# Optimization experiments

Measured on AMD Instinct MI355X. Metric: run time of the kernel, lower is better.

Reference implementation:

```python
import jax, jax.numpy as jnp
import numpy as np

MESSAGE_PASSES = 3  # constants.message_passes
F_NODE = 64   # hidden_node_features
F_EDGE = 16   # n_edge_features
M_MSG = 64    # message_size
OUT_DIM = 128
B, N = 8, 256
EDGE_DENSITY = 0.1


def setup_inputs() -> dict:
    key = jax.random.key(0)
    ks = jax.random.split(key, 12)
    nodes = jax.random.normal(ks[0], (B, N, F_NODE), dtype=jnp.float32)
    # sparse positive edge features: rand * bernoulli connectivity (avg degree ~ N*density)
    raw = jax.random.uniform(ks[1], (B, N, N, F_EDGE), dtype=jnp.float32)
    conn = (jax.random.uniform(ks[2], (B, N, N)) < EDGE_DENSITY).astype(jnp.float32)
    edges = raw * conn[..., None]
    s = 0.05
    return {
        "nodes": nodes,
        "edges": edges,
        # message MLP: cat(neighbour, edge) -> message_size
        "W_msg": jax.random.normal(ks[3], (F_NODE + F_EDGE, M_MSG), dtype=jnp.float32) * s,
        "b_msg": jnp.zeros((M_MSG,), dtype=jnp.float32),
        # GRU cell (input=message_size, hidden=F_NODE), gates [r|z|n]
        "W_i": jax.random.normal(ks[4], (M_MSG, 3 * F_NODE), dtype=jnp.float32) * s,
        "W_h": jax.random.normal(ks[5], (F_NODE, 3 * F_NODE), dtype=jnp.float32) * s,
        "b_i": jnp.zeros((3 * F_NODE,), dtype=jnp.float32),
        "b_h": jnp.zeros((3 * F_NODE,), dtype=jnp.float32),
        # gated readout
        "W_g": jax.random.normal(ks[6], (2 * F_NODE, OUT_DIM), dtype=jnp.float32) * s,
        "b_g": jnp.zeros((OUT_DIM,), dtype=jnp.float32),
        "W_e": jax.random.normal(ks[7], (F_NODE, OUT_DIM), dtype=jnp.float32) * s,
        "b_e": jnp.zeros((OUT_DIM,), dtype=jnp.float32),
    }


def reference(nodes, edges, W_msg, b_msg, W_i, W_h, b_i, b_h, W_g, b_g, W_e, b_e):
    # adjacency[b,i,j] != 0  <=>  edge (i<-j) exists (original: edges.sum(3).nonzero)
    adjacency = edges.sum(axis=-1)                                   # (B,N,N)
    nbr_mask = (adjacency != 0).astype(nodes.dtype)                  # (B,N,N)
    node_mask = (adjacency.sum(axis=-1) != 0)                        # (B,N) bool
    node_mask_f = node_mask.astype(nodes.dtype)

    h = nodes                                                        # hidden_nodes init = nodes
    b, n, f = nodes.shape
    for _ in range(MESSAGE_PASSES):
        # message_terms over all (node i, neighbour j) pairs; masked sum == padded-gather sum
        nghb = jnp.broadcast_to(h[:, None, :, :], (b, n, n, f))      # (B,N,N,F) neighbour feats
        feat = jnp.concatenate([nghb, edges], axis=-1)               # (B,N,N,F+E)
        terms = jax.nn.relu(feat @ W_msg + b_msg)                    # (B,N,N,M)
        messages = jnp.einsum('bijm,bij->bim', terms, nbr_mask)      # summation aggregation
        # GRU cell update
        gi = messages @ W_i + b_i                                    # (B,N,3F)
        gh = h @ W_h + b_h
        ir, iz, inn = jnp.split(gi, 3, axis=-1)
        hr, hz, hn = jnp.split(gh, 3, axis=-1)
        r = jax.nn.sigmoid(ir + hr)
        z = jax.nn.sigmoid(iz + hz)
        ng = jnp.tanh(inn + r * hn)
        h_new = (1.0 - z) * ng + z * h
        # only nodes with nonzero degree are scattered back (original indexes node_batch idc)
        h = jnp.where(node_mask[..., None], h_new, h)

    # gated readout: sum_i mask_i * sigmoid(g([h_i, x_i])) * e(h_i)
    gate = jax.nn.sigmoid(jnp.concatenate([h, nodes], axis=-1) @ W_g + b_g)  # (B,N,OUT)
    emb = h @ W_e + b_e                                                      # (B,N,OUT)
    out = jnp.einsum('bno,bn->bo', gate * emb, node_mask_f)                  # (B,OUT)
    return out
```

## Files before the change

kernel.cpp:

```cpp
#include <hip/hip_runtime.h>
#include <hip/hip_bf16.h>

#define BB 8
#define NN 256
#define FF 64
#define EE 16
#define MM 64
#define G3 192
#define OUTD 128
#define ROWS (BB*NN)
#define MAXD 64

__device__ __forceinline__ float sigmoidf_(float x) {
    return 1.0f / (1.0f + __expf(-x));
}

__global__ __launch_bounds__(256) void k_prep(
    const float* __restrict__ nodes, const float* __restrict__ edges,
    const float* __restrict__ Wmsg, const float* __restrict__ bmsg,
    int* __restrict__ deg, int* __restrict__ nbr,
    float* __restrict__ h, float* __restrict__ hn, float* __restrict__ out)
{
    int row = blockIdx.x;
    int tid = threadIdx.x;
    int lane = tid & 63, wv = tid >> 6;
    __shared__ int wcnt[4];
    __shared__ float snode[FF];

    const float4* ep = (const float4*)(edges + (((size_t)row) * NN + tid) * EE);
    float4 a = ep[0], b4 = ep[1], c4 = ep[2], d4 = ep[3];
    float s = a.x+a.y+a.z+a.w + b4.x+b4.y+b4.z+b4.w
            + c4.x+c4.y+c4.z+c4.w + d4.x+d4.y+d4.z+d4.w;
    bool pred = (s != 0.0f);
    unsigned long long m = __ballot(pred);
    if (lane == 0) wcnt[wv] = __popcll(m);
    if (tid < FF) snode[tid] = nodes[(size_t)row * FF + tid];
    __syncthreads();

    int base = 0;
    #pragma unroll
    for (int q = 0; q < 4; ++q) base += (q < wv) ? wcnt[q] : 0;
    int slot = base + __popcll(m & ((1ull << lane) - 1ull));
    if (pred && slot < MAXD) nbr[row * MAXD + slot] = tid;

    if (tid == 0) {
        int tot = wcnt[0] + wcnt[1] + wcnt[2] + wcnt[3];
        deg[row] = (tot < MAXD) ? tot : MAXD;
    }
    if (tid < FF) h[row * FF + tid] = snode[tid];
    if (tid < MM) {
        float acc = bmsg[tid];
        #pragma unroll 8
        for (int k = 0; k < FF; ++k) acc += snode[k] * Wmsg[k * MM + tid];
        hn[row * MM + tid] = acc;
    }
    if (row == 0) {
        #pragma unroll
        for (int i = 0; i < (BB * OUTD) / 256; ++i) out[i * 256 + tid] = 0.0f;
    }
}

__global__ __launch_bounds__(512, 8) void k_pass2(
    const float* __restrict__ edges,
    const float* __restrict__ Wmsg, const float* __restrict__ bmsg,
    const float* __restrict__ Wi, const float* __restrict__ Wh,
    const float* __restrict__ bi, const float* __restrict__ bh,
    const float* __restrict__ nodes,
    const float* __restrict__ Wg, const float* __restrict__ bg,
    const float* __restrict__ We, const float* __restrict__ be,
    const int* __restrict__ deg, const int* __restrict__ nbr,
    const float* __restrict__ hn_in, float* __restrict__ hn_out,
    float* __restrict__ h, float* __restrict__ out, int last)
{
    const int r0  = blockIdx.x * 2;
    const int b   = r0 >> 8;
    const int tid = threadIdx.x;
    const int w   = tid >> 6;
    const int lane = tid & 63;

    __shared__ int   snbr[2][MAXD];
    __shared__ int   sdeg[2];
    __shared__ float efeat[2][MAXD][EE];
    __shared__ float part[8][MM];
    __shared__ float smsg[2][MM];
    __shared__ float shold[2][FF];
    __shared__ float sx[2][FF];
    __shared__ float gI[2][3][FF], gH[2][3][FF];
    __shared__ float shnew[2][FF];
    __shared__ float sg[2][OUTD], se[2][OUTD];

    if (tid < 2) sdeg[tid] = deg[r0 + tid];
    if (tid < 2 * MAXD) {
        int r = tid >> 6;
        snbr[r][tid & 63] = nbr[(r0 + r) * MAXD + (tid & 63)];
    }
    if (tid < 2 * FF) {
        int r = tid >> 6;
        shold[r][tid & 63] = h[(size_t)(r0 + r) * FF + (tid & 63)];
    }
    if (last && tid >= 2 * FF && tid < 4 * FF) {
        int r = (tid >> 6) & 1;
        sx[r][tid & 63] = nodes[(size_t)(r0 + r) * FF + (tid & 63)];
    }

    float we[EE];
    #pragma unroll
    for (int k = 0; k < EE; ++k) we[k] = Wmsg[(FF + k) * MM + lane];
    __syncthreads();

    #pragma unroll
    for (int r = 0; r < 2; ++r) {
        int cnt = sdeg[r] * EE;
        for (int i = tid; i < cnt; i += 512) {
            int slot = i >> 4, k = i & 15;
            efeat[r][slot][k] = edges[(((size_t)(r0 + r)) * NN + snbr[r][slot]) * EE + k];
        }
    }
    __syncthreads();

    {
        int r = w >> 2, sub = w & 3;
        int d = sdeg[r];
        const float* hb = hn_in + (size_t)b * NN * MM;
        float acc = 0.0f;
        for (int s = sub; s < d; s += 4) {
            int j = snbr[r][s];
            float term = hb[j * MM + lane];
            #pragma unroll
            for (int k = 0; k < EE; ++k) term += efeat[r][s][k] * we[k];
            acc += fmaxf(term, 0.0f);
        }
        part[w][lane] = acc;
    }
    __syncthreads();
    if ((w & 3) == 0) {
        int r = w >> 2;
        smsg[r][lane] = part[w][lane] + part[w + 1][lane]
                      + part[w + 2][lane] + part[w + 3][lane];
    }
    __syncthreads();

    if (w < 3) {
        float a0 = bi[w * FF + lane], a1 = a0;
        #pragma unroll 4
        for (int k = 0; k < FF; ++k) {
            float wgt = Wi[k * G3 + w * FF + lane];
            a0 += smsg[0][k] * wgt;
            a1 += smsg[1][k] * wgt;
        }
        gI[0][w][lane] = a0; gI[1][w][lane] = a1;
    } else if (w < 6) {
        int g = w - 3;
        float a0 = bh[g * FF + lane], a1 = a0;
        #pragma unroll 4
        for (int k = 0; k < FF; ++k) {
            float wgt = Wh[k * G3 + g * FF + lane];
            a0 += shold[0][k] * wgt;
            a1 += shold[1][k] * wgt;
        }
        gH[0][g][lane] = a0; gH[1][g][lane] = a1;
    }
    __syncthreads();

    if (tid < 2 * FF) {
        int r = tid >> 6, tt = tid & 63;
        float rr = sigmoidf_(gI[r][0][tt] + gH[r][0][tt]);
        float zz = sigmoidf_(gI[r][1][tt] + gH[r][1][tt]);
        float ng = tanhf(gI[r][2][tt] + rr * gH[r][2][tt]);
        float hold = shold[r][tt];
        float hnew = (1.0f - zz) * ng + zz * hold;
        if (sdeg[r] == 0) hnew = hold;
        shnew[r][tt] = hnew;
        h[(size_t)(r0 + r) * FF + tt] = hnew;
    }
    __syncthreads();

    if (!last) {
        {
            int r = w >> 2, kq = w & 3;
            float p = 0.0f;
            #pragma unroll
            for (int kk = 0; kk < 16; ++kk) {
                int k = kq * 16 + kk;
                p += shnew[r][k] * Wmsg[k * MM + lane];
            }
            part[w][lane] = p;
        }
        __syncthreads();
        if (tid < 2 * MM) {
            int r = tid >> 6, tt = tid & 63;
            hn_out[(size_t)(r0 + r) * MM + tt] = bmsg[tt]
                + part[r*4+0][tt] + part[r*4+1][tt] + part[r*4+2][tt] + part[r*4+3][tt];
        }
    } else {
        int grp = tid >> 7, o = tid & 127;
        int r = grp >> 1, kind = grp & 1;
        if (kind == 0) {
            float g = bg[o];
            #pragma unroll 4
            for (int k = 0; k < FF; ++k) g += shnew[r][k] * Wg[k * OUTD + o];
            #pragma unroll 4
            for (int k = 0; k < FF; ++k) g += sx[r][k] * Wg[(FF + k) * OUTD + o];
            sg[r][o] = g;
        } else {
            float e = be[o];
            #pragma unroll 4
            for (int k = 0; k < FF; ++k) e += shnew[r][k] * We[k * OUTD + o];
            se[r][o] = e;
        }
        __syncthreads();
        if (tid < OUTD) {
            float v0 = (sdeg[0] != 0) ? sigmoidf_(sg[0][tid]) * se[0][tid] : 0.0f;
            float v1 = (sdeg[1] != 0) ? sigmoidf_(sg[1][tid]) * se[1][tid] : 0.0f;
            atomicAdd(&out[b * OUTD + tid], v0 + v1);
        }
    }
}

extern "C" void kernel_launch(void* const* d_in, const int* in_sizes, int n_in,
                              void* d_out, int out_size, void* d_ws, size_t ws_size,
                              hipStream_t stream) {
    const float* nodes = (const float*)d_in[0];
    const float* edges = (const float*)d_in[1];
    const float* Wmsg  = (const float*)d_in[2];
    const float* bmsg  = (const float*)d_in[3];
    const float* Wi    = (const float*)d_in[4];
    const float* Wh    = (const float*)d_in[5];
    const float* bi    = (const float*)d_in[6];
    const float* bh    = (const float*)d_in[7];
    const float* Wg    = (const float*)d_in[8];
    const float* bg    = (const float*)d_in[9];
    const float* We    = (const float*)d_in[10];
    const float* be    = (const float*)d_in[11];
    float* out = (float*)d_out;
    char* ws = (char*)d_ws;

    int*   deg  = (int*)ws;
    int*   nbr  = (int*)(ws + 8192);
    float* h    = (float*)(ws + 8192 + (size_t)ROWS * MAXD * 4);
    float* hnA  = h   + (size_t)ROWS * FF;
    float* hnB  = hnA + (size_t)ROWS * MM;

    k_prep<<<ROWS, 256, 0, stream>>>(nodes, edges, Wmsg, bmsg, deg, nbr, h, hnA, out);

    k_pass2<<<ROWS/2, 512, 0, stream>>>(edges, Wmsg, bmsg, Wi, Wh, bi, bh,
                                        nodes, Wg, bg, We, be, deg, nbr,
                                        hnA, hnB, h, out, 0);
    k_pass2<<<ROWS/2, 512, 0, stream>>>(edges, Wmsg, bmsg, Wi, Wh, bi, bh,
                                        nodes, Wg, bg, We, be, deg, nbr,
                                        hnB, hnA, h, out, 0);
    k_pass2<<<ROWS/2, 512, 0, stream>>>(edges, Wmsg, bmsg, Wi, Wh, bi, bh,
                                        nodes, Wg, bg, We, be, deg, nbr,
                                        hnA, hnB, h, out, 1);
}
```

Baseline: 144.5 us.

## Precompute edge-feature message projections once and process four rows per block

The prep kernel now stores each row's compacted edge features in shared memory and precomputes their projection through the edge half of W_msg into a workspace buffer (edot). The three pass kernels then read that buffer instead of re-gathering edges and recomputing the 16-term dot products every pass. Each pass block now handles four rows with 1024 threads, so Wi/Wh/Wmsg weight loads are shared across more rows and the gate matmuls are split across two K halves. The cost is a larger workspace (ROWS*64*64 floats) with extra global writes in prep and reads per pass, plus bigger blocks that may reduce occupancy flexibility.

After: 152.1 us. +5.2%, slower.

```diff
diff --git a/kernel.cpp b/kernel.cpp
--- a/kernel.cpp
+++ b/kernel.cpp
@@ -10,6 +10,7 @@
 #define OUTD 128
 #define ROWS (BB*NN)
 #define MAXD 64
+#define RPB 4
 
 __device__ __forceinline__ float sigmoidf_(float x) {
     return 1.0f / (1.0f + __expf(-x));
@@ -19,13 +20,16 @@
     const float* __restrict__ nodes, const float* __restrict__ edges,
     const float* __restrict__ Wmsg, const float* __restrict__ bmsg,
     int* __restrict__ deg, int* __restrict__ nbr,
-    float* __restrict__ h, float* __restrict__ hn, float* __restrict__ out)
+    float* __restrict__ h, float* __restrict__ hn,
+    float* __restrict__ edot, float* __restrict__ out)
 {
     int row = blockIdx.x;
     int tid = threadIdx.x;
     int lane = tid & 63, wv = tid >> 6;
     __shared__ int wcnt[4];
+    __shared__ int sdg;
     __shared__ float snode[FF];
+    __shared__ float efeat[MAXD][EE];
 
     const float4* ep = (const float4*)(edges + (((size_t)row) * NN + tid) * EE);
     float4 a = ep[0], b4 = ep[1], c4 = ep[2], d4 = ep[3];
@@ -41,12 +45,18 @@
     #pragma unroll
     for (int q = 0; q < 4; ++q) base += (q < wv) ? wcnt[q] : 0;
     int slot = base + __popcll(m & ((1ull << lane) - 1ull));
-    if (pred && slot < MAXD) nbr[row * MAXD + slot] = tid;
-
+    if (pred && slot < MAXD) {
+        nbr[row * MAXD + slot] = tid;
+        float4* dst = (float4*)&efeat[slot][0];
+        dst[0] = a; dst[1] = b4; dst[2] = c4; dst[3] = d4;
+    }
     if (tid == 0) {
         int tot = wcnt[0] + wcnt[1] + wcnt[2] + wcnt[3];
-        deg[row] = (tot < MAXD) ? tot : MAXD;
-    }
+        sdg = (tot < MAXD) ? tot : MAXD;
+        deg[row] = sdg;
+    }
+    __syncthreads();
+
     if (tid < FF) h[row * FF + tid] = snode[tid];
     if (tid < MM) {
         float acc = bmsg[tid];
@@ -54,14 +64,27 @@
         for (int k = 0; k < FF; ++k) acc += snode[k] * Wmsg[k * MM + tid];
         hn[row * MM + tid] = acc;
     }
+
+    float we[EE];
+    #pragma unroll
+    for (int k = 0; k < EE; ++k) we[k] = Wmsg[(FF + k) * MM + lane];
+
+    int d = sdg;
+    float* ed = edot + (size_t)row * MAXD * MM;
+    for (int sl = wv; sl < d; sl += 4) {
+        float acc = 0.0f;
+        #pragma unroll
+        for (int k = 0; k < EE; ++k) acc += efeat[sl][k] * we[k];
+        ed[sl * MM + lane] = acc;
+    }
+
     if (row == 0) {
         #pragma unroll
         for (int i = 0; i < (BB * OUTD) / 256; ++i) out[i * 256 + tid] = 0.0f;
     }
 }
 
-__global__ __launch_bounds__(512, 8) void k_pass2(
-    const float* __restrict__ edges,
+__global__ __launch_bounds__(1024, 8) void k_pass4(
     const float* __restrict__ Wmsg, const float* __restrict__ bmsg,
     const float* __restrict__ Wi, const float* __restrict__ Wh,
     const float* __restrict__ bi, const float* __restrict__ bh,
@@ -69,52 +92,35 @@
     const float* __restrict__ Wg, const float* __restrict__ bg,
     const float* __restrict__ We, const float* __restrict__ be,
     const int* __restrict__ deg, const int* __restrict__ nbr,
+    const float* __restrict__ edot,
     const float* __restrict__ hn_in, float* __restrict__ hn_out,
     float* __restrict__ h, float* __restrict__ out, int last)
 {
-    const int r0  = blockIdx.x * 2;
-    const int b   = r0 >> 8;
-    const int tid = threadIdx.x;
-    const int w   = tid >> 6;
+    const int r0   = blockIdx.x * RPB;
+    const int b    = r0 >> 8;
+    const int tid  = threadIdx.x;
+    const int w    = tid >> 6;
     const int lane = tid & 63;
 
-    __shared__ int   snbr[2][MAXD];
-    __shared__ int   sdeg[2];
-    __shared__ float efeat[2][MAXD][EE];
-    __shared__ float part[8][MM];
-    __shared__ float smsg[2][MM];
-    __shared__ float shold[2][FF];
-    __shared__ float sx[2][FF];
-    __shared__ float gI[2][3][FF], gH[2][3][FF];
-    __shared__ float shnew[2][FF];
-    __shared__ float sg[2][OUTD], se[2][OUTD];
-
-    if (tid < 2) sdeg[tid] = deg[r0 + tid];
-    if (tid < 2 * MAXD) {
-        int r = tid >> 6;
-        snbr[r][tid & 63] = nbr[(r0 + r) * MAXD + (tid & 63)];
-    }
-    if (tid < 2 * FF) {
-        int r = tid >> 6;
-        shold[r][tid & 63] = h[(size_t)(r0 + r) * FF + (tid & 63)];
-    }
-    if (last && tid >= 2 * FF && tid < 4 * FF) {
-        int r = (tid >> 6) & 1;
-        sx[r][tid & 63] = nodes[(size_t)(r0 + r) * FF + (tid & 63)];
-    }
-
-    float we[EE];
-    #pragma unroll
-    for (int k = 0; k < EE; ++k) we[k] = Wmsg[(FF + k) * MM + lane];
-    __syncthreads();
-
-    #pragma unroll
-    for (int r = 0; r < 2; ++r) {
-        int cnt = sdeg[r] * EE;
-        for (int i = tid; i < cnt; i += 512) {
-            int slot = i >> 4, k = i & 15;
-            efeat[r][slot][k] = edges[(((size_t)(r0 + r)) * NN + snbr[r][slot]) * EE + k];
-        }
+    __shared__ int   snbr[RPB][MAXD];
+    __shared__ int   sdeg[RPB];
+    __shared__ float part[16][MM];
+    __shared__ float smsg[RPB][MM];
+    __shared__ float sh[RPB][FF];
+    __shared__ float sx[RPB][FF];
+    __shared__ float pg[6][2][RPB][FF];
+    __shared__ float sg[RPB][OUTD];
+    __shared__ float se[RPB][OUTD];
+
+    if (tid < RPB) sdeg[tid] = deg[r0 + tid];
+    if (tid < RPB * MAXD) {
+        snbr[tid >> 6][tid & 63] = nbr[(r0 + (tid >> 6)) * MAXD + (tid & 63)];
+    } else if (tid < 2 * RPB * MAXD) {
+        int x = tid - RPB * MAXD;
+        sh[x >> 6][x & 63] = h[(size_t)(r0 + (x >> 6)) * FF + (x & 63)];
+    } else if (last && tid < 3 * RPB * MAXD) {
+        int x = tid - 2 * RPB * MAXD;
+        sx[x >> 6][x & 63] = nodes[(size_t)(r0 + (x >> 6)) * FF + (x & 63)];
     }
     __syncthreads();
 
@@ -122,75 +128,80 @@
         int r = w >> 2, sub = w & 3;
         int d = sdeg[r];
         const float* hb = hn_in + (size_t)b * NN * MM;
+        const float* ed = edot + (size_t)(r0 + r) * MAXD * MM;
         float acc = 0.0f;
         for (int s = sub; s < d; s += 4) {
             int j = snbr[r][s];
-            float term = hb[j * MM + lane];
-            #pragma unroll
-            for (int k = 0; k < EE; ++k) term += efeat[r][s][k] * we[k];
-            acc += fmaxf(term, 0.0f);
+            acc += fmaxf(hb[j * MM + lane] + ed[s * MM + lane], 0.0f);
         }
         part[w][lane] = acc;
     }
     __syncthreads();
-    if ((w & 3) == 0) {
-        int r = w >> 2;
-        smsg[r][lane] = part[w][lane] + part[w + 1][lane]
-                      + part[w + 2][lane] + part[w + 3][lane];
-    }
-    __syncthreads();
-
-    if (w < 3) {
-        float a0 = bi[w * FF + lane], a1 = a0;
-        #pragma unroll 4
-        for (int k = 0; k < FF; ++k) {
-            float wgt = Wi[k * G3 + w * FF + lane];
-            a0 += smsg[0][k] * wgt;
-            a1 += smsg[1][k] * wgt;
-        }
-        gI[0][w][lane] = a0; gI[1][w][lane] = a1;
-    } else if (w < 6) {
-        int g = w - 3;
-        float a0 = bh[g * FF + lane], a1 = a0;
-        #pragma unroll 4
-        for (int k = 0; k < FF; ++k) {
-            float wgt = Wh[k * G3 + g * FF + lane];
-            a0 += shold[0][k] * wgt;
-            a1 += shold[1][k] * wgt;
-        }
-        gH[0][g][lane] = a0; gH[1][g][lane] = a1;
-    }
-    __syncthreads();
-
-    if (tid < 2 * FF) {
+    if (tid < RPB * MM) {
         int r = tid >> 6, tt = tid & 63;
-        float rr = sigmoidf_(gI[r][0][tt] + gH[r][0][tt]);
-        float zz = sigmoidf_(gI[r][1][tt] + gH[r][1][tt]);
-        float ng = tanhf(gI[r][2][tt] + rr * gH[r][2][tt]);
-        float hold = shold[r][tt];
+        smsg[r][tt] = part[r*4][tt] + part[r*4+1][tt] + part[r*4+2][tt] + part[r*4+3][tt];
+    }
+    __syncthreads();
+
+    if (w < 12) {
+        int g = w >> 1, kh = w & 1;
+        float a0 = 0, a1 = 0, a2 = 0, a3 = 0;
+        if (g < 3) {
+            for (int k = kh * 32; k < kh * 32 + 32; ++k) {
+                float wgt = Wi[k * G3 + g * FF + lane];
+                a0 += smsg[0][k] * wgt; a1 += smsg[1][k] * wgt;
+                a2 += smsg[2][k] * wgt; a3 += smsg[3][k] * wgt;
+            }
+        } else {
+            int gg = g - 3;
+            for (int k = kh * 32; k < kh * 32 + 32; ++k) {
+                float wgt = Wh[k * G3 + gg * FF + lane];
+                a0 += sh[0][k] * wgt; a1 += sh[1][k] * wgt;
+                a2 += sh[2][k] * wgt; a3 += sh[3][k] * wgt;
+            }
+        }
+        pg[g][kh][0][lane] = a0; pg[g][kh][1][lane] = a1;
+        pg[g][kh][2][lane] = a2; pg[g][kh][3][lane] = a3;
+    }
+    __syncthreads();
+
+    if (tid < RPB * FF) {
+        int r = tid >> 6, tt = tid & 63;
+        float ir  = bi[tt]          + pg[0][0][r][tt] + pg[0][1][r][tt];
+        float iz  = bi[FF + tt]     + pg[1][0][r][tt] + pg[1][1][r][tt];
+        float in_ = bi[2*FF + tt]   + pg[2][0][r][tt] + pg[2][1][r][tt];
+        float hr  = bh[tt]          + pg[3][0][r][tt] + pg[3][1][r][tt];
+        float hz  = bh[FF + tt]     + pg[4][0][r][tt] + pg[4][1][r][tt];
+        float hnn = bh[2*FF + tt]   + pg[5][0][r][tt] + pg[5][1][r][tt];
+        float rr = sigmoidf_(ir + hr);
+        float zz = sigmoidf_(iz + hz);
+        float ng = tanhf(in_ + rr * hnn);
+        float hold = sh[r][tt];
         float hnew = (1.0f - zz) * ng + zz * hold;
         if (sdeg[r] == 0) hnew = hold;
-        shnew[r][tt] = hnew;
-        h[(size_t)(r0 + r) * FF + tt] = hnew;
+        sh[r][tt] = hnew;
+        if (!last) h[(size_t)(r0 + r) * FF + tt] = hnew;
     }
     __syncthreads();
 
     if (!last) {
-        {
-            int r = w >> 2, kq = w & 3;
-            float p = 0.0f;
+        if (w < 4) {
+            float a0 = 0, a1 = 0, a2 = 0, a3 = 0;
             #pragma unroll
             for (int kk = 0; kk < 16; ++kk) {
-                int k = kq * 16 + kk;
-                p += shnew[r][k] * Wmsg[k * MM + lane];
+                int k = w * 16 + kk;
+                float wgt = Wmsg[k * MM + lane];
+                a0 += sh[0][k] * wgt; a1 += sh[1][k] * wgt;
+                a2 += sh[2][k] * wgt; a3 += sh[3][k] * wgt;
             }
-            part[w][lane] = p;
+            part[w*4+0][lane] = a0; part[w*4+1][lane] = a1;
+            part[w*4+2][lane] = a2; part[w*4+3][lane] = a3;
         }
         __syncthreads();
-        if (tid < 2 * MM) {
+        if (tid < RPB * MM) {
             int r = tid >> 6, tt = tid & 63;
             hn_out[(size_t)(r0 + r) * MM + tt] = bmsg[tt]
-                + part[r*4+0][tt] + part[r*4+1][tt] + part[r*4+2][tt] + part[r*4+3][tt];
+                + part[0*4+r][tt] + part[1*4+r][tt] + part[2*4+r][tt] + part[3*4+r][tt];
         }
     } else {
         int grp = tid >> 7, o = tid & 127;
@@ -198,21 +209,23 @@
         if (kind == 0) {
             float g = bg[o];
             #pragma unroll 4
-            for (int k = 0; k < FF; ++k) g += shnew[r][k] * Wg[k * OUTD + o];
+            for (int k = 0; k < FF; ++k) g += sh[r][k] * Wg[k * OUTD + o];
             #pragma unroll 4
             for (int k = 0; k < FF; ++k) g += sx[r][k] * Wg[(FF + k) * OUTD + o];
             sg[r][o] = g;
         } else {
             float e = be[o];
             #pragma unroll 4
-            for (int k = 0; k < FF; ++k) e += shnew[r][k] * We[k * OUTD + o];
+            for (int k = 0; k < FF; ++k) e += sh[r][k] * We[k * OUTD + o];
             se[r][o] = e;
         }
         __syncthreads();
         if (tid < OUTD) {
-            float v0 = (sdeg[0] != 0) ? sigmoidf_(sg[0][tid]) * se[0][tid] : 0.0f;
-            float v1 = (sdeg[1] != 0) ? sigmoidf_(sg[1][tid]) * se[1][tid] : 0.0f;
-            atomicAdd(&out[b * OUTD + tid], v0 + v1);
+            float v = 0.0f;
+            #pragma unroll
+            for (int r2 = 0; r2 < RPB; ++r2)
+                v += (sdeg[r2] != 0) ? sigmoidf_(sg[r2][tid]) * se[r2][tid] : 0.0f;
+            atomicAdd(&out[b * OUTD + tid], v);
         }
     }
 }
@@ -238,18 +251,20 @@
     int*   deg  = (int*)ws;
     int*   nbr  = (int*)(ws + 8192);
     float* h    = (float*)(ws + 8192 + (size_t)ROWS * MAXD * 4);
-    float* hnA  = h   + (size_t)ROWS * FF;
-    float* hnB  = hnA + (size_t)ROWS * MM;
-
-    k_prep<<<ROWS, 256, 0, stream>>>(nodes, edges, Wmsg, bmsg, deg, nbr, h, hnA, out);
-
-    k_pass2<<<ROWS/2, 512, 0, stream>>>(edges, Wmsg, bmsg, Wi, Wh, bi, bh,
-                                        nodes, Wg, bg, We, be, deg, nbr,
-                                        hnA, hnB, h, out, 0);
-    k_pass2<<<ROWS/2, 512, 0, stream>>>(edges, Wmsg, bmsg, Wi, Wh, bi, bh,
-                                        nodes, Wg, bg, We, be, deg, nbr,
-                                        hnB, hnA, h, out, 0);
-    k_pass2<<<ROWS/2, 512, 0, stream>>>(edges, Wmsg, bmsg, Wi, Wh, bi, bh,
-                                        nodes, Wg, bg, We, be, deg, nbr,
-                                        hnA, hnB, h, out, 1);
-}
+    float* hnA  = h    + (size_t)ROWS * FF;
+    float* hnB  = hnA  + (size_t)ROWS * MM;
+    float* edot = hnB  + (size_t)ROWS * MM;
+
+    k_prep<<<ROWS, 256, 0, stream>>>(nodes, edges, Wmsg, bmsg, deg, nbr,
+                                     h, hnA, edot, out);
+
+    k_pass4<<<ROWS/RPB, 1024, 0, stream>>>(Wmsg, bmsg, Wi, Wh, bi, bh,
+                                           nodes, Wg, bg, We, be, deg, nbr, edot,
+                                           hnA, hnB, h, out, 0);
+    k_pass4<<<ROWS/RPB, 1024, 0, stream>>>(Wmsg, bmsg, Wi, Wh, bi, bh,
+                                           nodes, Wg, bg, We, be, deg, nbr, edot,
+                                           hnB, hnA, h, out, 0);
+    k_pass4<<<ROWS/RPB, 1024, 0, stream>>>(Wmsg, bmsg, Wi, Wh, bi, bh,
+                                           nodes, Wg, bg, We, be, deg, nbr, edot,
+                                           hnA, hnB, h, out, 1);
+}
```
